# Performance work log

Hardware: AMD Instinct MI355X
Metric: run time of the kernel (lower is better)

Reference implementation:

```python
import jax, jax.numpy as jnp
import numpy as np

MAXL = 16      # max_chunk_length (hardcoded in forward)
MAXC = 1024    # max_num_chuncks (hardcoded in forward)
D = 128        # hidden_dim
SENT = 2**30   # sentinel 'end' for non-boundary positions


def setup_inputs() -> dict:
    key = jax.random.key(0)
    k1, k2, k3, k4, k5 = jax.random.split(key, 5)
    B, S = 8, 8192
    x = jax.random.normal(k1, (B, S, D), jnp.float32)
    pad_token_vector = jax.random.normal(k2, (D,), jnp.float32)
    x_ids = jax.random.randint(k3, (B, S), 0, 32000, jnp.int32)
    # end_of_seq_head params: Linear(128, 2, bias=True)
    W = jax.random.normal(k4, (D, 2), jnp.float32) * 0.1
    b = jax.random.normal(k5, (2,), jnp.float32) * 0.1
    return {"x": x, "pad_token_vector": pad_token_vector, "x_ids": x_ids,
            "pad_token_id": 0, "W": W, "b": b}


def _chunk_one(x_i, ids_i, logits_i, pad_vec, pad_id):
    # x_i: (S, D), ids_i: (S,), logits_i: (S, 2)
    S = x_i.shape[0]
    boundary = logits_i[:-1, 0] > logits_i[:-1, 1]          # (S-1,)
    pos = jnp.arange(S - 1, dtype=jnp.int32)

    # Sequential recurrence: prev_idx advances at boundaries, clipped to MAXL per chunk.
    def step(carry, inp):
        prev, cnt = carry
        bnd, ii = inp
        event = bnd & (cnt < MAXC)
        nxt = jnp.minimum(prev + MAXL, ii + 1)
        prev2 = jnp.where(event, nxt, prev)
        end = jnp.where(event, nxt, jnp.int32(SENT))
        return (prev2, cnt + event.astype(jnp.int32)), end

    (final_prev, _), ends = jax.lax.scan(
        step, (jnp.int32(0), jnp.int32(0)), (boundary, pos))
    # Chunk e consumes tokens [cum_end[e-1], cum_end[e]); ends of real events are
    # strictly increasing, sentinels sort to the back.
    ends = jnp.sort(ends)
    t = jnp.arange(S, dtype=jnp.int32)
    cid = jnp.searchsorted(ends, t, side='right').astype(jnp.int32)   # chunk id per token
    start = jnp.where(cid > 0, ends[jnp.maximum(cid - 1, 0)], 0)
    consumed = t < final_prev
    flat = jnp.where(consumed, cid * MAXL + (t - start), MAXC * MAXL)  # dump slot for pads

    # Source inits buffer to ones*pad_vec then does `+=`, so written cells = pad + x.
    buf = jnp.zeros((MAXC * MAXL + 1, D), x_i.dtype).at[flat].add(x_i)
    out = pad_vec + buf[:-1].reshape(MAXC, MAXL, D)
    idb = jnp.full((MAXC * MAXL + 1,), pad_id, jnp.float32).at[flat].set(
        ids_i.astype(jnp.float32))
    return out, idb[:-1].reshape(MAXC, MAXL)


def reference(x, pad_token_vector, x_ids, pad_token_id, W, b):
    # NOTE: source applies end_of_seq_head to the ORIGINAL x; the 2 transformer
    # blocks write x_chunking which is never used (dead code) -> omitted.
    logits = x @ W + b                                       # (B, S, 2)
    f = lambda xi, ii, li: _chunk_one(xi, ii, li, pad_token_vector, pad_token_id)
    output_tensor, output_token_ids = jax.vmap(f)(x, x_ids, logits)
    return output_tensor, output_token_ids
```

## Files before the change

### kernel.cpp

```cpp
#include <hip/hip_runtime.h>
#include <hip/hip_bf16.h>
#include <climits>

#define S 8192
#define D_DIM 128
#define MAXL 16
#define MAXC 1024
#define NB 8

__global__ __launch_bounds__(256) void bnd_kernel(
    const float* __restrict__ x, const float* __restrict__ W,
    const float* __restrict__ bias, unsigned char* __restrict__ bnd) {
  int gtid = blockIdx.x * 256 + threadIdx.x;
  int wid = gtid >> 6;
  int lane = threadIdx.x & 63;
  int sub = lane >> 4;
  int fg = lane & 15;
  int row = wid * 4 + sub;
  bool valid = row < NB * (S - 1);
  double d = 0.0;
  int b = 0, t = 0;
  if (valid) {
    b = row / (S - 1);
    t = row - b * (S - 1);
    const float* xr = x + ((size_t)b * S + t) * D_DIM + fg * 8;
    float4 xa = ((const float4*)xr)[0];
    float4 xb = ((const float4*)xr)[1];
    const float* wr = W + fg * 16;
    float4 w0 = ((const float4*)wr)[0];
    float4 w1 = ((const float4*)wr)[1];
    float4 w2 = ((const float4*)wr)[2];
    float4 w3 = ((const float4*)wr)[3];
    d += (double)xa.x * ((double)w0.x - (double)w0.y);
    d += (double)xa.y * ((double)w0.z - (double)w0.w);
    d += (double)xa.z * ((double)w1.x - (double)w1.y);
    d += (double)xa.w * ((double)w1.z - (double)w1.w);
    d += (double)xb.x * ((double)w2.x - (double)w2.y);
    d += (double)xb.y * ((double)w2.z - (double)w2.w);
    d += (double)xb.z * ((double)w3.x - (double)w3.y);
    d += (double)xb.w * ((double)w3.z - (double)w3.w);
  }
  for (int m = 1; m < 16; m <<= 1) d += __shfl_xor(d, m, 64);
  if (valid && fg == 0) {
    double thr = (double)bias[1] - (double)bias[0];
    bnd[b * S + t] = (d > thr) ? 1 : 0;
  }
}

__global__ __launch_bounds__(1024) void scan_kernel(
    const unsigned char* __restrict__ bnd, int* __restrict__ ends,
    int* __restrict__ numEv) {
  int b = blockIdx.x;
  int tid = threadIdx.x;
  int lane = tid & 63;
  int wv = tid >> 6;
  __shared__ int wsum[16];
  __shared__ int wmin[16];
  __shared__ int evpos[1024];
  __shared__ int s_total;

  const unsigned char* bb = bnd + b * S;
  unsigned long long w = *(const unsigned long long*)(bb + tid * 8);
  if (tid == 1023) w &= 0x00FFFFFFFFFFFFFFull;
  unsigned long long bits = w & 0x0101010101010101ull;
  int cnt = __popcll(bits);

  int inc = cnt;
  for (int off = 1; off < 64; off <<= 1) {
    int v = __shfl_up(inc, off, 64);
    if (lane >= off) inc += v;
  }
  if (lane == 63) wsum[wv] = inc;
  __syncthreads();
  if (wv == 0 && lane < 16) {
    int v = wsum[lane];
    int iv = v;
    for (int off = 1; off < 16; off <<= 1) {
      int u = __shfl_up(iv, off, 64);
      if (lane >= off) iv += u;
    }
    if (lane == 15) s_total = iv;
    wsum[lane] = iv - v;
  }
  __syncthreads();
  int excl = wsum[wv] + inc - cnt;

  int idx = excl;
#pragma unroll
  for (int i = 0; i < 8; ++i) {
    if ((w >> (8 * i)) & 1ull) {
      if (idx < MAXC) evpos[idx] = tid * 8 + i;
      idx++;
    }
  }
  __syncthreads();
  int total = s_total;
  int nev = total < MAXC ? total : MAXC;

  int g = (tid < nev) ? (evpos[tid] + 1 - MAXL * tid) : INT_MAX;
  int incm = g;
  for (int off = 1; off < 64; off <<= 1) {
    int v = __shfl_up(incm, off, 64);
    if (lane >= off) incm = incm < v ? incm : v;
  }
  if (lane == 63) wmin[wv] = incm;
  __syncthreads();
  if (wv == 0 && lane < 16) {
    int iv = wmin[lane];
    for (int off = 1; off < 16; off <<= 1) {
      int u = __shfl_up(iv, off, 64);
      if (lane >= off) iv = iv < u ? iv : u;
    }
    int ex = __shfl_up(iv, 1, 64);
    if (lane == 0) ex = INT_MAX;
    wmin[lane] = ex;
  }
  __syncthreads();
  int wex = wmin[wv];
  int m = incm < wex ? incm : wex;

  if (tid < nev) {
    int cap = m < MAXL ? m : MAXL;
    ends[b * MAXC + tid] = MAXL * tid + cap;
  }
  if (tid == 0) numEv[b] = nev;
}

__global__ __launch_bounds__(256) void out_kernel(
    const float* __restrict__ x, const float* __restrict__ pad,
    const int* __restrict__ xids, const int* __restrict__ pad_id,
    const int* __restrict__ ends, const int* __restrict__ numEv,
    float* __restrict__ out_t, float* __restrict__ out_ids) {
  int gid = blockIdx.x * 256 + threadIdx.x;
  int row = gid >> 5;
  int q = gid & 31;
  int b = row >> 14;
  int rem = row & 16383;
  int c = rem >> 4;
  int l = rem & 15;
  int nev = numEv[b];
  int tok = -1;
  if (c < nev) {
    int e = ends[b * MAXC + c];
    int s = c ? ends[b * MAXC + c - 1] : 0;
    if (l < e - s) tok = s + l;
  }
  float4 o = ((const float4*)pad)[q];
  if (tok >= 0) {
    float4 xv = ((const float4*)(x + ((size_t)(b * S + tok)) * D_DIM))[q];
    o.x += xv.x; o.y += xv.y; o.z += xv.z; o.w += xv.w;
  }
  ((float4*)out_t)[(size_t)row * 32 + q] = o;
  if (q == 0) {
    out_ids[row] = (tok >= 0) ? (float)xids[b * S + tok] : (float)(*pad_id);
  }
}

extern "C" void kernel_launch(void* const* d_in, const int* in_sizes, int n_in,
                              void* d_out, int out_size, void* d_ws, size_t ws_size,
                              hipStream_t stream) {
  const float* x = (const float*)d_in[0];
  const float* pad_vec = (const float*)d_in[1];
  const int* x_ids = (const int*)d_in[2];
  const int* pad_id = (const int*)d_in[3];
  const float* W = (const float*)d_in[4];
  const float* bias = (const float*)d_in[5];

  unsigned char* bnd = (unsigned char*)d_ws;
  int* ends = (int*)((char*)d_ws + NB * S);
  int* numEv = (int*)((char*)d_ws + NB * S + NB * MAXC * 4);

  float* out_t = (float*)d_out;
  float* out_ids = out_t + (size_t)NB * MAXC * MAXL * D_DIM;

  int rows = NB * (S - 1);
  int waves = (rows + 3) / 4;
  int blocksA = (waves * 64 + 255) / 256;
  hipLaunchKernelGGL(bnd_kernel, dim3(blocksA), dim3(256), 0, stream,
                     x, W, bias, bnd);

  hipLaunchKernelGGL(scan_kernel, dim3(NB), dim3(1024), 0, stream,
                     bnd, ends, numEv);

  int out_rows = NB * MAXC * MAXL;
  int blocksC = out_rows / 8;
  hipLaunchKernelGGL(out_kernel, dim3(blocksC), dim3(256), 0, stream,
                     x, pad_vec, x_ids, pad_id, ends, numEv, out_t, out_ids);
}
```

Before: 112.5 us.

## Fuse boundary detection and per-batch scan via last-block-done atomic counter

Merges the boundary-logit kernel and the per-batch scan kernel into one launch. Each block bumps a per-batch atomic counter after writing its boundary bytes, and whichever block finishes last for a batch runs that batch's scan with 256 threads, each handling 4 words. The aim is to drop one kernel launch and the serialization gap between the two stages. In exchange it adds a memset launch, atomics and threadfences, and the scan now runs on a smaller 256-thread block.

```diff
diff --git a/kernel.cpp b/kernel.cpp
--- a/kernel.cpp
+++ b/kernel.cpp
@@ -7,17 +7,20 @@
 #define MAXL 16
 #define MAXC 1024
 #define NB 8
-
-__global__ __launch_bounds__(256) void bnd_kernel(
+#define ROWS (NB * (S - 1))
+#define ROWS_PER_BLK 16
+
+__global__ __launch_bounds__(256) void bnd_scan_kernel(
     const float* __restrict__ x, const float* __restrict__ W,
-    const float* __restrict__ bias, unsigned char* __restrict__ bnd) {
-  int gtid = blockIdx.x * 256 + threadIdx.x;
-  int wid = gtid >> 6;
-  int lane = threadIdx.x & 63;
+    const float* __restrict__ bias, unsigned char* __restrict__ bnd,
+    int* __restrict__ ends, int* __restrict__ numEv, int* __restrict__ cnt_) {
+  int tid = threadIdx.x;
+  int lane = tid & 63;
+  int wv = tid >> 6;
   int sub = lane >> 4;
   int fg = lane & 15;
-  int row = wid * 4 + sub;
-  bool valid = row < NB * (S - 1);
+  int row = blockIdx.x * ROWS_PER_BLK + wv * 4 + sub;
+  bool valid = row < ROWS;
   double d = 0.0;
   int b = 0, t = 0;
   if (valid) {
@@ -45,85 +48,120 @@
     double thr = (double)bias[1] - (double)bias[0];
     bnd[b * S + t] = (d > thr) ? 1 : 0;
   }
-}
-
-__global__ __launch_bounds__(1024) void scan_kernel(
-    const unsigned char* __restrict__ bnd, int* __restrict__ ends,
-    int* __restrict__ numEv) {
-  int b = blockIdx.x;
-  int tid = threadIdx.x;
-  int lane = tid & 63;
-  int wv = tid >> 6;
-  __shared__ int wsum[16];
-  __shared__ int wmin[16];
-  __shared__ int evpos[1024];
+
+  __shared__ int doscan[2];
+  __shared__ int sbatch[2];
+  __syncthreads();
+  if (tid == 0) {
+    __threadfence();
+    int r0 = blockIdx.x * ROWS_PER_BLK;
+    int r1 = r0 + ROWS_PER_BLK - 1;
+    if (r1 > ROWS - 1) r1 = ROWS - 1;
+    int b0 = r0 / (S - 1);
+    int b1 = r1 / (S - 1);
+    doscan[0] = doscan[1] = 0;
+    sbatch[0] = b0; sbatch[1] = b1;
+    int nb = (b1 > b0) ? 2 : 1;
+    for (int k = 0; k < nb; ++k) {
+      int bb = (k == 0) ? b0 : b1;
+      int first = (bb * (S - 1)) / ROWS_PER_BLK;
+      int last = (bb * (S - 1) + S - 2) / ROWS_PER_BLK;
+      int tgt = last - first + 1;
+      int old = atomicAdd(&cnt_[bb], 1);
+      if (old == tgt - 1) doscan[k] = 1;
+    }
+  }
+  __syncthreads();
+  if (!(doscan[0] | doscan[1])) return;
+
+  __shared__ int evpos[MAXC];
+  __shared__ int wsum[4];
+  __shared__ int wmin[4];
   __shared__ int s_total;
 
-  const unsigned char* bb = bnd + b * S;
-  unsigned long long w = *(const unsigned long long*)(bb + tid * 8);
-  if (tid == 1023) w &= 0x00FFFFFFFFFFFFFFull;
-  unsigned long long bits = w & 0x0101010101010101ull;
-  int cnt = __popcll(bits);
-
-  int inc = cnt;
-  for (int off = 1; off < 64; off <<= 1) {
-    int v = __shfl_up(inc, off, 64);
-    if (lane >= off) inc += v;
-  }
-  if (lane == 63) wsum[wv] = inc;
-  __syncthreads();
-  if (wv == 0 && lane < 16) {
-    int v = wsum[lane];
-    int iv = v;
-    for (int off = 1; off < 16; off <<= 1) {
-      int u = __shfl_up(iv, off, 64);
-      if (lane >= off) iv += u;
-    }
-    if (lane == 15) s_total = iv;
-    wsum[lane] = iv - v;
-  }
-  __syncthreads();
-  int excl = wsum[wv] + inc - cnt;
-
-  int idx = excl;
-#pragma unroll
-  for (int i = 0; i < 8; ++i) {
-    if ((w >> (8 * i)) & 1ull) {
-      if (idx < MAXC) evpos[idx] = tid * 8 + i;
-      idx++;
-    }
-  }
-  __syncthreads();
-  int total = s_total;
-  int nev = total < MAXC ? total : MAXC;
-
-  int g = (tid < nev) ? (evpos[tid] + 1 - MAXL * tid) : INT_MAX;
-  int incm = g;
-  for (int off = 1; off < 64; off <<= 1) {
-    int v = __shfl_up(incm, off, 64);
-    if (lane >= off) incm = incm < v ? incm : v;
-  }
-  if (lane == 63) wmin[wv] = incm;
-  __syncthreads();
-  if (wv == 0 && lane < 16) {
-    int iv = wmin[lane];
-    for (int off = 1; off < 16; off <<= 1) {
-      int u = __shfl_up(iv, off, 64);
-      if (lane >= off) iv = iv < u ? iv : u;
-    }
-    int ex = __shfl_up(iv, 1, 64);
-    if (lane == 0) ex = INT_MAX;
-    wmin[lane] = ex;
-  }
-  __syncthreads();
-  int wex = wmin[wv];
-  int m = incm < wex ? incm : wex;
-
-  if (tid < nev) {
-    int cap = m < MAXL ? m : MAXL;
-    ends[b * MAXC + tid] = MAXL * tid + cap;
-  }
-  if (tid == 0) numEv[b] = nev;
+  for (int k = 0; k < 2; ++k) {
+    if (!doscan[k]) continue;
+    if (k == 1 && doscan[0] && sbatch[1] == sbatch[0]) continue;
+    int bb = sbatch[k];
+    __threadfence();
+    const unsigned long long* p = (const unsigned long long*)(bnd + bb * S);
+    unsigned long long w[4];
+#pragma unroll
+    for (int i = 0; i < 4; ++i) w[i] = p[4 * tid + i];
+    if (tid == 255) w[3] &= 0x00FFFFFFFFFFFFFFull;
+    int cnt = 0;
+#pragma unroll
+    for (int i = 0; i < 4; ++i)
+      cnt += __popcll(w[i] & 0x0101010101010101ull);
+
+    int inc = cnt;
+    for (int off = 1; off < 64; off <<= 1) {
+      int v = __shfl_up(inc, off, 64);
+      if (lane >= off) inc += v;
+    }
+    if (lane == 63) wsum[wv] = inc;
+    __syncthreads();
+    if (tid == 0) {
+      int a = 0;
+#pragma unroll
+      for (int i = 0; i < 4; ++i) { int v = wsum[i]; wsum[i] = a; a += v; }
+      s_total = a;
+    }
+    __syncthreads();
+    int excl = wsum[wv] + inc - cnt;
+
+    int idx = excl;
+#pragma unroll
+    for (int i = 0; i < 4; ++i) {
+      unsigned long long wi = w[i];
+      for (int j = 0; j < 8; ++j) {
+        if ((wi >> (8 * j)) & 1ull) {
+          if (idx < MAXC) evpos[idx] = tid * 32 + i * 8 + j;
+          idx++;
+        }
+      }
+    }
+    __syncthreads();
+    int total = s_total;
+    int nev = total < MAXC ? total : MAXC;
+
+    int m[4];
+    int run = INT_MAX;
+#pragma unroll
+    for (int i = 0; i < 4; ++i) {
+      int j = 4 * tid + i;
+      int g = (j < nev) ? (evpos[j] + 1 - MAXL * j) : INT_MAX;
+      run = run < g ? run : g;
+      m[i] = run;
+    }
+    int incm = run;
+    for (int off = 1; off < 64; off <<= 1) {
+      int v = __shfl_up(incm, off, 64);
+      if (lane >= off) incm = incm < v ? incm : v;
+    }
+    if (lane == 63) wmin[wv] = incm;
+    __syncthreads();
+    if (tid == 0) {
+      int a = INT_MAX;
+#pragma unroll
+      for (int i = 0; i < 4; ++i) { int v = wmin[i]; wmin[i] = a; a = a < v ? a : v; }
+    }
+    __syncthreads();
+    int exm = __shfl_up(incm, 1, 64);
+    if (lane == 0) exm = INT_MAX;
+    int pre = wmin[wv] < exm ? wmin[wv] : exm;
+#pragma unroll
+    for (int i = 0; i < 4; ++i) {
+      int j = 4 * tid + i;
+      if (j < nev) {
+        int cum = pre < m[i] ? pre : m[i];
+        int cap = cum < MAXL ? cum : MAXL;
+        ends[bb * MAXC + j] = MAXL * j + cap;
+      }
+    }
+    if (tid == 0) numEv[bb] = nev;
+    __syncthreads();
+  }
 }
 
 __global__ __launch_bounds__(256) void out_kernel(
@@ -169,18 +207,16 @@
   unsigned char* bnd = (unsigned char*)d_ws;
   int* ends = (int*)((char*)d_ws + NB * S);
   int* numEv = (int*)((char*)d_ws + NB * S + NB * MAXC * 4);
+  int* cnt_ = (int*)((char*)d_ws + NB * S + NB * MAXC * 4 + NB * 4);
 
   float* out_t = (float*)d_out;
   float* out_ids = out_t + (size_t)NB * MAXC * MAXL * D_DIM;
 
-  int rows = NB * (S - 1);
-  int waves = (rows + 3) / 4;
-  int blocksA = (waves * 64 + 255) / 256;
-  hipLaunchKernelGGL(bnd_kernel, dim3(blocksA), dim3(256), 0, stream,
-                     x, W, bias, bnd);
-
-  hipLaunchKernelGGL(scan_kernel, dim3(NB), dim3(1024), 0, stream,
-                     bnd, ends, numEv);
+  hipMemsetAsync(cnt_, 0, NB * sizeof(int), stream);
+
+  int blocksA = (ROWS + ROWS_PER_BLK - 1) / ROWS_PER_BLK;
+  hipLaunchKernelGGL(bnd_scan_kernel, dim3(blocksA), dim3(256), 0, stream,
+                     x, W, bias, bnd, ends, numEv, cnt_);
 
   int out_rows = NB * MAXC * MAXL;
   int blocksC = out_rows / 8;
```

Result: slower. 224.8 us (+99.9%).
